# Performance work log

Hardware: AMD Instinct MI355X
Metric: run time of the kernel (lower is better)

The kernel has to match this reference:

```python
import jax, jax.numpy as jnp
import numpy as np

N, T, F, HID, HEADS, E = 10000, 6, 64, 64, 4, 160000


def gat_conv(x, W, a_src, a_dst, bias, src, dst, n, concat):
    """PyG-style GATConv (self-loops already appended to src/dst).
    x: [n, in]; W: [in, H*C]; a_src/a_dst: [H, C]; returns ([n, H*C] or [n, C], alpha [E', H])."""
    H, C = a_src.shape
    xw = (x @ W).reshape(n, H, C)
    # per-edge unnormalized attention logits
    al = (xw * a_src).sum(-1)[src] + (xw * a_dst).sum(-1)[dst]  # [E', H]
    al = jax.nn.leaky_relu(al, 0.2)
    # segment softmax over destination neighborhoods
    m = jax.ops.segment_max(al, dst, num_segments=n)
    ex = jnp.exp(al - m[dst])
    s = jax.ops.segment_sum(ex, dst, num_segments=n)
    alpha = ex / (s[dst] + 1e-16)
    out = jax.ops.segment_sum(xw[src] * alpha[:, :, None], dst, num_segments=n)  # [n, H, C]
    out = out.reshape(n, H * C) if concat else out.mean(axis=1)
    return out + bias, alpha


def setup_inputs() -> dict:
    key = jax.random.key(0)
    ks = jax.random.split(key, 12)
    sc = 0.05
    return {
        "x": jax.random.normal(ks[0], (N, T, F), jnp.float32),
        "edge_index": jax.random.randint(ks[1], (2, E), 0, N, jnp.int64),
        "W0": jax.random.normal(ks[2], (F, HID), jnp.float32) * sc,
        "a_src0": jax.random.normal(ks[3], (HEADS, HID // HEADS), jnp.float32) * sc,
        "a_dst0": jax.random.normal(ks[4], (HEADS, HID // HEADS), jnp.float32) * sc,
        "b0": jnp.zeros((HID,), jnp.float32),
        "W1": jax.random.normal(ks[5], (HID, HEADS * HID), jnp.float32) * sc,
        "a_src1": jax.random.normal(ks[6], (HEADS, HID), jnp.float32) * sc,
        "a_dst1": jax.random.normal(ks[7], (HEADS, HID), jnp.float32) * sc,
        "b1": jnp.zeros((HID,), jnp.float32),
        "ln_g": jnp.ones((HID,), jnp.float32),
        "ln_b": jnp.zeros((HID,), jnp.float32),
        "W_ih": jax.random.normal(ks[8], (3 * HID, HID), jnp.float32) * sc,
        "W_hh": jax.random.normal(ks[9], (3 * HID, HID), jnp.float32) * sc,
        "b_ih": jnp.zeros((3 * HID,), jnp.float32),
        "b_hh": jnp.zeros((3 * HID,), jnp.float32),
    }


def reference(x, edge_index, W0, a_src0, a_dst0, b0, W1, a_src1, a_dst1, b1,
              ln_g, ln_b, W_ih, W_hh, b_ih, b_hh):
    n = x.shape[0]
    loops = jnp.arange(n)
    src = jnp.concatenate([edge_index[0], loops])  # add self loops
    dst = jnp.concatenate([edge_index[1], loops])

    def gat_step(_, xt):
        h, _a = gat_conv(xt, W0, a_src0, a_dst0, b0, src, dst, n, True)
        h = jax.nn.elu(h)  # dropout is identity in eval mode
        h, alpha = gat_conv(h, W1, a_src1, a_dst1, b1, src, dst, n, False)
        h = jax.nn.elu(h)
        mu = h.mean(-1, keepdims=True)
        v = ((h - mu) ** 2).mean(-1, keepdims=True)
        h = (h - mu) / jnp.sqrt(v + 1e-5) * ln_g + ln_b
        return None, (h, alpha)

    _, (Hs, alphas) = jax.lax.scan(gat_step, None, jnp.moveaxis(x, 1, 0))  # Hs: [T, n, HID]

    def gru_step(h, xt):
        gi = xt @ W_ih.T + b_ih
        gh = h @ W_hh.T + b_hh
        ir, iz, ig = jnp.split(gi, 3, axis=-1)
        hr, hz, hg = jnp.split(gh, 3, axis=-1)
        r = jax.nn.sigmoid(ir + hr)
        z = jax.nn.sigmoid(iz + hz)
        g = jnp.tanh(ig + r * hg)
        return (1.0 - z) * g + z * h, None

    h0 = jnp.zeros((n, W_hh.shape[1]), x.dtype)
    hT, _ = jax.lax.scan(gru_step, h0, Hs)  # last GRU output == last hidden (1 layer)
    attn_edge_index = jnp.stack([src, dst])
    return hT, alphas[-1], attn_edge_index
```

## Files before the change

kernel.cpp:

```cpp
#include <hip/hip_runtime.h>
#include <hip/hip_bf16.h>
#include <cstdint>
#include <cstddef>

#define N_NODES 10000
#define T_STEPS 6
#define F_IN    64
#define HID     64
#define HEADS   4
#define E_EDGES 160000
#define EP      (E_EDGES + N_NODES)
#define TN      (T_STEPS * N_NODES)
#define NTILES  (TN / 16)

typedef __hip_bfloat16 bf16;
typedef __attribute__((ext_vector_type(8))) short short8;
typedef __attribute__((ext_vector_type(4))) float floatx4;

__device__ __forceinline__ float bfu(unsigned short s) { return __uint_as_float((unsigned)s << 16); }
__device__ __forceinline__ unsigned short f2bu(float f) {
    bf16 b = __float2bfloat16(f);
    return *(unsigned short*)&b;
}
__device__ __forceinline__ void lds_fence() {
    asm volatile("s_waitcnt lgkmcnt(0)" ::: "memory");
}


__global__ void k_count(const int* ei, int* counts) {
    int e = blockIdx.x * blockDim.x + threadIdx.x;
    if (e >= EP) return;
    int dst = (e < E_EDGES) ? ei[E_EDGES + e] : (e - E_EDGES);
    atomicAdd(&counts[dst], 1);
}

__global__ void k_scan(const int* counts, int* rowstart) {
    __shared__ int part[1024];
    int tid = threadIdx.x;
    const int chunk = (N_NODES + 1023) / 1024;
    int base = tid * chunk;
    int s = 0;
    for (int i = 0; i < chunk; i++) { int idx = base + i; if (idx < N_NODES) s += counts[idx]; }
    part[tid] = s;
    __syncthreads();
    for (int off = 1; off < 1024; off <<= 1) {
        int v = (tid >= off) ? part[tid - off] : 0;
        __syncthreads();
        part[tid] += v;
        __syncthreads();
    }
    int run = (tid == 0) ? 0 : part[tid - 1];
    for (int i = 0; i < chunk; i++) {
        int idx = base + i;
        if (idx < N_NODES) { rowstart[idx] = run; run += counts[idx]; }
    }
    if (tid == 0) rowstart[N_NODES] = EP;
}

__global__ void k_scatter(const int* ei, const int* rowstart, int* fill,
                          int* csr_src, int* csr_eid, float* out_ei) {
    int e = blockIdx.x * blockDim.x + threadIdx.x;
    if (e >= EP) return;
    int src = (e < E_EDGES) ? ei[e] : (e - E_EDGES);
    int dst = (e < E_EDGES) ? ei[E_EDGES + e] : (e - E_EDGES);
    int pos = rowstart[dst] + atomicAdd(&fill[dst], 1);
    csr_src[pos] = src;
    csr_eid[pos] = e;
    out_ei[e] = (float)src;
    out_ei[EP + e] = (float)dst;
}


__global__ __launch_bounds__(256) void k_prep(const float* __restrict__ W0,
                                              const float* __restrict__ W1,
                                              const float* __restrict__ a_src0,
                                              const float* __restrict__ a_dst0,
                                              const float* __restrict__ a_src1,
                                              const float* __restrict__ a_dst1,
                                              const float* __restrict__ W_ih,
                                              const float* __restrict__ W_hh,
                                              bf16* __restrict__ W0bt,
                                              bf16* __restrict__ W1bt,
                                              bf16* __restrict__ wihb,
                                              bf16* __restrict__ whhb,
                                              float* __restrict__ P0s,
                                              float* __restrict__ P0d,
                                              float* __restrict__ P1s,
                                              float* __restrict__ P1d) {
    int b = blockIdx.x, tid = threadIdx.x;
    if (b == 176) {
        int h = tid >> 6, k = tid & 63;
        float ps = 0.f, pd = 0.f;
        for (int c = 0; c < 64; c++) {
            float wv = W1[k * 256 + h * 64 + c];
            ps += wv * a_src1[h * 64 + c];
            pd += wv * a_dst1[h * 64 + c];
        }
        P1s[h * 64 + k] = ps;
        P1d[h * 64 + k] = pd;
        return;
    }
    if (b == 177) {
        int h = tid >> 6, k = tid & 63;
        float ps = 0.f, pd = 0.f;
        for (int c = 0; c < 16; c++) {
            float wv = W0[k * 64 + h * 16 + c];
            ps += wv * a_src0[h * 16 + c];
            pd += wv * a_dst0[h * 16 + c];
        }
        P0s[h * 64 + k] = ps;
        P0d[h * 64 + k] = pd;
        return;
    }
    int i = b * 256 + tid;
    if (i < 4096) {
        W0bt[i] = __float2bfloat16(W0[(i & 63) * 64 + (i >> 6)]);
    } else if (i < 20480) {
        int j = i - 4096; int c = j >> 8, K = j & 255;
        W1bt[j] = __float2bfloat16(W1[(K & 63) * 256 + (K >> 6) * 64 + c]);
    } else if (i < 32768) {
        wihb[i - 20480] = __float2bfloat16(W_ih[i - 20480]);
    } else {
        whhb[i - 32768] = __float2bfloat16(W_hh[i - 32768]);
    }
}

__global__ __launch_bounds__(256) void k_gemm0(const float* __restrict__ x,
                                               const bf16* __restrict__ W0bt,
                                               const float* __restrict__ P0s,
                                               const float* __restrict__ P0d,
                                               bf16* __restrict__ XW0b,
                                               float* __restrict__ ALS0,
                                               float* __restrict__ ALD0) {
    __shared__ __align__(16) bf16 wt[64 * 64];
    int tid = threadIdx.x;
    for (int i = tid; i < 512; i += 256)
        ((short8*)wt)[i] = ((const short8*)W0bt)[i];
    __syncthreads();
    int wv = tid >> 6, lane = tid & 63;
    int tile = blockIdx.x * 4 + wv;
    if (tile >= NTILES) return;
    int rb = tile * 16;
    int m = lane & 15, quad = lane >> 4;
    int row = rb + m;
    int t = row / N_NODES, n = row - t * N_NODES;
    const float* xr = x + ((size_t)n * T_STEPS + t) * F_IN + quad * 8;
    short8 a0, a1;
#pragma unroll
    for (int j = 0; j < 8; j++) {
        a0[j] = (short)f2bu(xr[j]);
        a1[j] = (short)f2bu(xr[32 + j]);
    }
    floatx4 acc[4];
#pragma unroll
    for (int ct = 0; ct < 4; ct++) {
        short8 bb0 = *(const short8*)(wt + (ct * 16 + m) * 64 + quad * 8);
        short8 bb1 = *(const short8*)(wt + (ct * 16 + m) * 64 + 32 + quad * 8);
        floatx4 a = {0.f, 0.f, 0.f, 0.f};
        a = __builtin_amdgcn_mfma_f32_16x16x32_bf16(a0, bb0, a, 0, 0, 0);
        a = __builtin_amdgcn_mfma_f32_16x16x32_bf16(a1, bb1, a, 0, 0, 0);
        acc[ct] = a;
    }
    short8 p0, p1;
#pragma unroll
    for (int j = 0; j < 8; j++) {
        int k0 = quad * 8 + j, k1 = 32 + quad * 8 + j;
        float v0 = 0.f, v1 = 0.f;
        if (m < 4)      { v0 = P0s[m * 64 + k0];       v1 = P0s[m * 64 + k1]; }
        else if (m < 8) { v0 = P0d[(m - 4) * 64 + k0]; v1 = P0d[(m - 4) * 64 + k1]; }
        p0[j] = (short)f2bu(v0);
        p1[j] = (short)f2bu(v1);
    }
    floatx4 ac5 = {0.f, 0.f, 0.f, 0.f};
    ac5 = __builtin_amdgcn_mfma_f32_16x16x32_bf16(a0, p0, ac5, 0, 0, 0);
    ac5 = __builtin_amdgcn_mfma_f32_16x16x32_bf16(a1, p1, ac5, 0, 0, 0);
#pragma unroll
    for (int ct = 0; ct < 4; ct++)
#pragma unroll
        for (int r = 0; r < 4; r++)
            XW0b[(size_t)(rb + quad * 4 + r) * 64 + ct * 16 + m] = __float2bfloat16(acc[ct][r]);
#pragma unroll
    for (int r = 0; r < 4; r++) {
        int orow = rb + quad * 4 + r;
        if (m < 4)      ALS0[orow * 4 + m] = ac5[r];
        else if (m < 8) ALD0[orow * 4 + (m - 4)] = ac5[r];
    }
}

__global__ __launch_bounds__(256) void k_fused0(const int* __restrict__ rowst,
                                                const int* __restrict__ csr_src,
                                                const bf16* __restrict__ XW0b,
                                                const float* __restrict__ ALS0,
                                                const float* __restrict__ ALD0,
                                                const float* __restrict__ b0,
                                                const float* __restrict__ P1s,
                                                const float* __restrict__ P1d,
                                                bf16* __restrict__ H0b,
                                                float* __restrict__ ALS1,
                                                float* __restrict__ ALD1) {
    __shared__ float exv[4][4][65][4];
    __shared__ int   srcs[4][4][68];
    int tid = threadIdx.x;
    int wv = tid >> 6, lane = tid & 63;
    int sub = lane >> 4, il = lane & 15;
    int wid = (blockIdx.x * 4 + wv) * 4 + sub;
    int t = wid / N_NODES, n = wid - t * N_NODES;
    int rs = rowst[n], re = rowst[n + 1];
    int deg = re - rs;
    int tb = t * N_NODES;
    int hsel = il >> 2;
    float4 ad = *(const float4*)(ALD0 + (size_t)wid * 4);
    float s0 = 0.f, s1 = 0.f, s2 = 0.f, s3 = 0.f;
    float a0 = 0.f, a1 = 0.f, a2 = 0.f, a3 = 0.f;
    float i0, i1, i2, i3;
    const bf16* hrow = XW0b + (size_t)tb * 64 + il * 4;

    if (deg <= 64) {
        int srcv[4];
#pragma unroll
        for (int b = 0; b < 4; b++) {
            int idx = b * 16 + il;
            srcv[b] = csr_src[idx < deg ? rs + idx : rs];
        }
        float4 asv[4];
#pragma unroll
        for (int b = 0; b < 4; b++)
            asv[b] = *(const float4*)(ALS0 + (size_t)(tb + srcv[b]) * 4);
#pragma unroll
        for (int b = 0; b < 4; b++) {
            int idx = b * 16 + il;
            bool valid = idx < deg;
            float l0 = asv[b].x + ad.x; l0 = l0 > 0.f ? l0 : 0.2f * l0;
            float l1 = asv[b].y + ad.y; l1 = l1 > 0.f ? l1 : 0.2f * l1;
            float l2 = asv[b].z + ad.z; l2 = l2 > 0.f ? l2 : 0.2f * l2;
            float l3 = asv[b].w + ad.w; l3 = l3 > 0.f ? l3 : 0.2f * l3;
            float e0 = valid ? __expf(fminf(l0, 80.f)) : 0.f;
            float e1 = valid ? __expf(fminf(l1, 80.f)) : 0.f;
            float e2 = valid ? __expf(fminf(l2, 80.f)) : 0.f;
            float e3 = valid ? __expf(fminf(l3, 80.f)) : 0.f;
            s0 += e0; s1 += e1; s2 += e2; s3 += e3;
            float4 ex4; ex4.x = e0; ex4.y = e1; ex4.z = e2; ex4.w = e3;
            *(float4*)&exv[wv][sub][idx][0] = ex4;
            srcs[wv][sub][idx] = srcv[b];
        }
#pragma unroll
        for (int o = 1; o <= 8; o <<= 1) {
            s0 += __shfl_xor(s0, o, 64); s1 += __shfl_xor(s1, o, 64);
            s2 += __shfl_xor(s2, o, 64); s3 += __shfl_xor(s3, o, 64);
        }
        i0 = 1.f / (s0 + 1e-16f); i1 = 1.f / (s1 + 1e-16f);
        i2 = 1.f / (s2 + 1e-16f); i3 = 1.f / (s3 + 1e-16f);
        lds_fence();
        int k = 0;
        for (; k + 4 <= deg; k += 4) {
            float axq[4]; int sxq[4];
#pragma unroll
            for (int j = 0; j < 4; j++) {
                axq[j] = exv[wv][sub][k + j][hsel];
                sxq[j] = srcs[wv][sub][k + j];
            }
            ushort4 uq[4];
#pragma unroll
            for (int j = 0; j < 4; j++)
                uq[j] = *(const ushort4*)(hrow + (size_t)sxq[j] * 64);
#pragma unroll
            for (int j = 0; j < 4; j++) {
                a0 += axq[j] * bfu(uq[j].x); a1 += axq[j] * bfu(uq[j].y);
                a2 += axq[j] * bfu(uq[j].z); a3 += axq[j] * bfu(uq[j].w);
            }
        }
        for (; k < deg; k++) {
            float aex = exv[wv][sub][k][hsel];
            int sx = srcs[wv][sub][k];
            ushort4 u = *(const ushort4*)(hrow + (size_t)sx * 64);
            a0 += aex * bfu(u.x); a1 += aex * bfu(u.y);
            a2 += aex * bfu(u.z); a3 += aex * bfu(u.w);
        }
    } else {
        for (int idx = il; idx < deg; idx += 16) {
            int src = csr_src[rs + idx];
            float4 as = *(const float4*)(ALS0 + (size_t)(tb + src) * 4);
            float l0 = as.x + ad.x; l0 = l0 > 0.f ? l0 : 0.2f * l0; s0 += __expf(fminf(l0, 80.f));
            float l1 = as.y + ad.y; l1 = l1 > 0.f ? l1 : 0.2f * l1; s1 += __expf(fminf(l1, 80.f));
            float l2 = as.z + ad.z; l2 = l2 > 0.f ? l2 : 0.2f * l2; s2 += __expf(fminf(l2, 80.f));
            float l3 = as.w + ad.w; l3 = l3 > 0.f ? l3 : 0.2f * l3; s3 += __expf(fminf(l3, 80.f));
        }
#pragma unroll
        for (int o = 1; o <= 8; o <<= 1) {
            s0 += __shfl_xor(s0, o, 64); s1 += __shfl_xor(s1, o, 64);
            s2 += __shfl_xor(s2, o, 64); s3 += __shfl_xor(s3, o, 64);
        }
        i0 = 1.f / (s0 + 1e-16f); i1 = 1.f / (s1 + 1e-16f);
        i2 = 1.f / (s2 + 1e-16f); i3 = 1.f / (s3 + 1e-16f);
        for (int cb = 0; cb < deg; cb += 64) {
            int cend = min(64, deg - cb);
            lds_fence();
            for (int q = 0; q < 64; q += 16) {
                int idx = q + il;
                bool valid = idx < cend;
                int src = csr_src[valid ? (rs + cb + idx) : rs];
                float4 as = *(const float4*)(ALS0 + (size_t)(tb + src) * 4);
                float l0 = as.x + ad.x; l0 = l0 > 0.f ? l0 : 0.2f * l0;
                float l1 = as.y + ad.y; l1 = l1 > 0.f ? l1 : 0.2f * l1;
                float l2 = as.z + ad.z; l2 = l2 > 0.f ? l2 : 0.2f * l2;
                float l3 = as.w + ad.w; l3 = l3 > 0.f ? l3 : 0.2f * l3;
                float4 ex4;
                ex4.x = valid ? __expf(fminf(l0, 80.f)) : 0.f;
                ex4.y = valid ? __expf(fminf(l1, 80.f)) : 0.f;
                ex4.z = valid ? __expf(fminf(l2, 80.f)) : 0.f;
                ex4.w = valid ? __expf(fminf(l3, 80.f)) : 0.f;
                *(float4*)&exv[wv][sub][idx][0] = ex4;
                srcs[wv][sub][idx] = src;
            }
            lds_fence();
            for (int k = 0; k < cend; k++) {
                float aex = exv[wv][sub][k][hsel];
                int sx = srcs[wv][sub][k];
                ushort4 u = *(const ushort4*)(hrow + (size_t)sx * 64);
                a0 += aex * bfu(u.x); a1 += aex * bfu(u.y);
                a2 += aex * bfu(u.z); a3 += aex * bfu(u.w);
            }
        }
    }
    float ih = (hsel == 0) ? i0 : (hsel == 1) ? i1 : (hsel == 2) ? i2 : i3;
    float4 bv = *(const float4*)(b0 + il * 4);
    float v0 = a0 * ih + bv.x; v0 = v0 > 0.f ? v0 : (__expf(v0) - 1.f);
    float v1 = a1 * ih + bv.y; v1 = v1 > 0.f ? v1 : (__expf(v1) - 1.f);
    float v2 = a2 * ih + bv.z; v2 = v2 > 0.f ? v2 : (__expf(v2) - 1.f);
    float v3 = a3 * ih + bv.w; v3 = v3 > 0.f ? v3 : (__expf(v3) - 1.f);
    ushort4 o4;
    o4.x = f2bu(v0); o4.y = f2bu(v1); o4.z = f2bu(v2); o4.w = f2bu(v3);
    *(ushort4*)(H0b + (size_t)wid * 64 + il * 4) = o4;

    float ps[4], pd[4];
#pragma unroll
    for (int h = 0; h < 4; h++) {
        float4 s4 = *(const float4*)(P1s + h * 64 + il * 4);
        float4 d4 = *(const float4*)(P1d + h * 64 + il * 4);
        ps[h] = v0 * s4.x + v1 * s4.y + v2 * s4.z + v3 * s4.w;
        pd[h] = v0 * d4.x + v1 * d4.y + v2 * d4.z + v3 * d4.w;
    }
#pragma unroll
    for (int o = 1; o <= 8; o <<= 1) {
#pragma unroll
        for (int h = 0; h < 4; h++) {
            ps[h] += __shfl_xor(ps[h], o, 64);
            pd[h] += __shfl_xor(pd[h], o, 64);
        }
    }
    if (il == 0) {
        float4 w1; w1.x = ps[0]; w1.y = ps[1]; w1.z = ps[2]; w1.w = ps[3];
        *(float4*)(ALS1 + (size_t)wid * 4) = w1;
        float4 w2; w2.x = pd[0]; w2.y = pd[1]; w2.z = pd[2]; w2.w = pd[3];
        *(float4*)(ALD1 + (size_t)wid * 4) = w2;
    }
}

__global__ __launch_bounds__(256) void k_fused1(const int* __restrict__ rowst,
                                                const int* __restrict__ csr_src,
                                                const int* __restrict__ csr_eid,
                                                const bf16* __restrict__ H0b,
                                                const float* __restrict__ ALS1,
                                                const float* __restrict__ ALD1,
                                                const bf16* __restrict__ W1bt,
                                                const float* __restrict__ b1,
                                                const float* __restrict__ ln_g,
                                                const float* __restrict__ ln_b,
                                                bf16* __restrict__ HSb,
                                                float* __restrict__ out_alpha) {
    __shared__ __align__(16) union SM {
        struct { float exv[4][4][65][4]; int srcs[4][4][68]; } p;
        struct { bf16 ast[16][264]; float ost[16][68]; } q;
    } sm;
    int tid = threadIdx.x;
    int wv = tid >> 6, lane = tid & 63;
    int sub = lane >> 4, il = lane & 15;
    int wid = (blockIdx.x * 4 + wv) * 4 + sub;
    int t = wid / N_NODES, n = wid - t * N_NODES;
    int rs = rowst[n], re = rowst[n + 1];
    int deg = re - rs;
    int tb = t * N_NODES;
    bool do_out = (t == T_STEPS - 1);
    float4 ad = *(const float4*)(ALD1 + (size_t)wid * 4);
    float s0 = 0.f, s1 = 0.f, s2 = 0.f, s3 = 0.f;
    float acc[4][4];
#pragma unroll
    for (int hh = 0; hh < 4; hh++)
#pragma unroll
        for (int j = 0; j < 4; j++) acc[hh][j] = 0.f;
    float i0, i1, i2, i3;
    const bf16* hrow = H0b + (size_t)tb * 64 + il * 4;

    if (deg <= 64) {
        int srcv[4];
#pragma unroll
        for (int b = 0; b < 4; b++) {
            int idx = b * 16 + il;
            srcv[b] = csr_src[idx < deg ? rs + idx : rs];
        }
        float4 asv[4];
#pragma unroll
        for (int b = 0; b < 4; b++)
            asv[b] = *(const float4*)(ALS1 + (size_t)(tb + srcv[b]) * 4);
#pragma unroll
        for (int b = 0; b < 4; b++) {
            int idx = b * 16 + il;
            bool valid = idx < deg;
            float l0 = asv[b].x + ad.x; l0 = l0 > 0.f ? l0 : 0.2f * l0;
            float l1 = asv[b].y + ad.y; l1 = l1 > 0.f ? l1 : 0.2f * l1;
            float l2 = asv[b].z + ad.z; l2 = l2 > 0.f ? l2 : 0.2f * l2;
            float l3 = asv[b].w + ad.w; l3 = l3 > 0.f ? l3 : 0.2f * l3;
            float e0 = valid ? __expf(fminf(l0, 80.f)) : 0.f;
            float e1 = valid ? __expf(fminf(l1, 80.f)) : 0.f;
            float e2 = valid ? __expf(fminf(l2, 80.f)) : 0.f;
            float e3 = valid ? __expf(fminf(l3, 80.f)) : 0.f;
            s0 += e0; s1 += e1; s2 += e2; s3 += e3;
            float4 ex4; ex4.x = e0; ex4.y = e1; ex4.z = e2; ex4.w = e3;
            *(float4*)&sm.p.exv[wv][sub][idx][0] = ex4;
            sm.p.srcs[wv][sub][idx] = srcv[b];
        }
#pragma unroll
        for (int o = 1; o <= 8; o <<= 1) {
            s0 += __shfl_xor(s0, o, 64); s1 += __shfl_xor(s1, o, 64);
            s2 += __shfl_xor(s2, o, 64); s3 += __shfl_xor(s3, o, 64);
        }
        i0 = 1.f / (s0 + 1e-16f); i1 = 1.f / (s1 + 1e-16f);
        i2 = 1.f / (s2 + 1e-16f); i3 = 1.f / (s3 + 1e-16f);
        lds_fence();
        if (do_out) {
            for (int b = 0; b < deg; b += 16) {
                int idx = b + il;
                if (idx < deg) {
                    int eid = csr_eid[rs + idx];
                    float4 ex4 = *(const float4*)&sm.p.exv[wv][sub][idx][0];
                    float4 o4;
                    o4.x = ex4.x * i0; o4.y = ex4.y * i1;
                    o4.z = ex4.z * i2; o4.w = ex4.w * i3;
                    *(float4*)(out_alpha + (size_t)eid * 4) = o4;
                }
            }
        }
        int k = 0;
        for (; k + 4 <= deg; k += 4) {
            float4 exq[4]; int sxq[4];
#pragma unroll
            for (int j = 0; j < 4; j++) {
                exq[j] = *(const float4*)&sm.p.exv[wv][sub][k + j][0];
                sxq[j] = sm.p.srcs[wv][sub][k + j];
            }
            ushort4 uq[4];
#pragma unroll
            for (int j = 0; j < 4; j++)
                uq[j] = *(const ushort4*)(hrow + (size_t)sxq[j] * 64);
#pragma unroll
            for (int j = 0; j < 4; j++) {
                float x0 = bfu(uq[j].x), x1 = bfu(uq[j].y), x2 = bfu(uq[j].z), x3 = bfu(uq[j].w);
                acc[0][0] += exq[j].x * x0; acc[0][1] += exq[j].x * x1; acc[0][2] += exq[j].x * x2; acc[0][3] += exq[j].x * x3;
                acc[1][0] += exq[j].y * x0; acc[1][1] += exq[j].y * x1; acc[1][2] += exq[j].y * x2; acc[1][3] += exq[j].y * x3;
                acc[2][0] += exq[j].z * x0; acc[2][1] += exq[j].z * x1; acc[2][2] += exq[j].z * x2; acc[2][3] += exq[j].z * x3;
                acc[3][0] += exq[j].w * x0; acc[3][1] += exq[j].w * x1; acc[3][2] += exq[j].w * x2; acc[3][3] += exq[j].w * x3;
            }
        }
        for (; k < deg; k++) {
            float4 ex = *(const float4*)&sm.p.exv[wv][sub][k][0];
            int sx = sm.p.srcs[wv][sub][k];
            ushort4 u = *(const ushort4*)(hrow + (size_t)sx * 64);
            float x0 = bfu(u.x), x1 = bfu(u.y), x2 = bfu(u.z), x3 = bfu(u.w);
            acc[0][0] += ex.x * x0; acc[0][1] += ex.x * x1; acc[0][2] += ex.x * x2; acc[0][3] += ex.x * x3;
            acc[1][0] += ex.y * x0; acc[1][1] += ex.y * x1; acc[1][2] += ex.y * x2; acc[1][3] += ex.y * x3;
            acc[2][0] += ex.z * x0; acc[2][1] += ex.z * x1; acc[2][2] += ex.z * x2; acc[2][3] += ex.z * x3;
            acc[3][0] += ex.w * x0; acc[3][1] += ex.w * x1; acc[3][2] += ex.w * x2; acc[3][3] += ex.w * x3;
        }
    } else {
        for (int idx = il; idx < deg; idx += 16) {
            int src = csr_src[rs + idx];
            float4 as = *(const float4*)(ALS1 + (size_t)(tb + src) * 4);
            float l0 = as.x + ad.x; l0 = l0 > 0.f ? l0 : 0.2f * l0; s0 += __expf(fminf(l0, 80.f));
            float l1 = as.y + ad.y; l1 = l1 > 0.f ? l1 : 0.2f * l1; s1 += __expf(fminf(l1, 80.f));
            float l2 = as.z + ad.z; l2 = l2 > 0.f ? l2 : 0.2f * l2; s2 += __expf(fminf(l2, 80.f));
            float l3 = as.w + ad.w; l3 = l3 > 0.f ? l3 : 0.2f * l3; s3 += __expf(fminf(l3, 80.f));
        }
#pragma unroll
        for (int o = 1; o <= 8; o <<= 1) {
            s0 += __shfl_xor(s0, o, 64); s1 += __shfl_xor(s1, o, 64);
            s2 += __shfl_xor(s2, o, 64); s3 += __shfl_xor(s3, o, 64);
        }
        i0 = 1.f / (s0 + 1e-16f); i1 = 1.f / (s1 + 1e-16f);
        i2 = 1.f / (s2 + 1e-16f); i3 = 1.f / (s3 + 1e-16f);
        for (int cb = 0; cb < deg; cb += 64) {
            int cend = min(64, deg - cb);
            lds_fence();
            for (int q = 0; q < 64; q += 16) {
                int idx = q + il;
                bool valid = idx < cend;
                int e = rs + cb + idx;
                int src = csr_src[valid ? e : rs];
                float4 as = *(const float4*)(ALS1 + (size_t)(tb + src) * 4);
                float l0 = as.x + ad.x; l0 = l0 > 0.f ? l0 : 0.2f * l0;
                float l1 = as.y + ad.y; l1 = l1 > 0.f ? l1 : 0.2f * l1;
                float l2 = as.z + ad.z; l2 = l2 > 0.f ? l2 : 0.2f * l2;
                float l3 = as.w + ad.w; l3 = l3 > 0.f ? l3 : 0.2f * l3;
                float e0 = valid ? __expf(fminf(l0, 80.f)) : 0.f;
                float e1 = valid ? __expf(fminf(l1, 80.f)) : 0.f;
                float e2 = valid ? __expf(fminf(l2, 80.f)) : 0.f;
                float e3 = valid ? __expf(fminf(l3, 80.f)) : 0.f;
                float4 ex4; ex4.x = e0; ex4.y = e1; ex4.z = e2; ex4.w = e3;
                *(float4*)&sm.p.exv[wv][sub][idx][0] = ex4;
                sm.p.srcs[wv][sub][idx] = src;
                if (do_out && valid) {
                    int eid = csr_eid[e];
                    float4 o4;
                    o4.x = e0 * i0; o4.y = e1 * i1; o4.z = e2 * i2; o4.w = e3 * i3;
                    *(float4*)(out_alpha + (size_t)eid * 4) = o4;
                }
            }
            lds_fence();
            for (int k = 0; k < cend; k++) {
                float4 ex = *(const float4*)&sm.p.exv[wv][sub][k][0];
                int sx = sm.p.srcs[wv][sub][k];
                ushort4 u = *(const ushort4*)(hrow + (size_t)sx * 64);
                float x0 = bfu(u.x), x1 = bfu(u.y), x2 = bfu(u.z), x3 = bfu(u.w);
                acc[0][0] += ex.x * x0; acc[0][1] += ex.x * x1; acc[0][2] += ex.x * x2; acc[0][3] += ex.x * x3;
                acc[1][0] += ex.y * x0; acc[1][1] += ex.y * x1; acc[1][2] += ex.y * x2; acc[1][3] += ex.y * x3;
                acc[2][0] += ex.z * x0; acc[2][1] += ex.z * x1; acc[2][2] += ex.z * x2; acc[2][3] += ex.z * x3;
                acc[3][0] += ex.w * x0; acc[3][1] += ex.w * x1; acc[3][2] += ex.w * x2; acc[3][3] += ex.w * x3;
            }
        }
    }
    float iv[4] = { i0, i1, i2, i3 };

    __syncthreads();
    int r_local = wv * 4 + sub;
#pragma unroll
    for (int hh = 0; hh < 4; hh++) {
        ushort4 o4;
        o4.x = f2bu(acc[hh][0] * iv[hh]); o4.y = f2bu(acc[hh][1] * iv[hh]);
        o4.z = f2bu(acc[hh][2] * iv[hh]); o4.w = f2bu(acc[hh][3] * iv[hh]);
        *(ushort4*)&sm.q.ast[r_local][hh * 64 + il * 4] = o4;
    }
    __syncthreads();
    int m = il, quad = sub;
    floatx4 ga = {0.f, 0.f, 0.f, 0.f};
    const bf16* wrow = W1bt + (size_t)(wv * 16 + m) * 256 + quad * 8;
#pragma unroll
    for (int kb = 0; kb < 8; kb++) {
        short8 afk = *(const short8*)&sm.q.ast[m][kb * 32 + quad * 8];
        short8 bfk = *(const short8*)(wrow + kb * 32);
        ga = __builtin_amdgcn_mfma_f32_16x16x32_bf16(afk, bfk, ga, 0, 0, 0);
    }
#pragma unroll
    for (int r = 0; r < 4; r++)
        sm.q.ost[quad * 4 + r][wv * 16 + m] = ga[r];
    __syncthreads();
    int row = wv * 4 + quad;
    float4 vv = *(const float4*)&sm.q.ost[row][m * 4];
    float4 bb = *(const float4*)(b1 + m * 4);
    float v0 = vv.x * 0.25f + bb.x; v0 = v0 > 0.f ? v0 : (__expf(v0) - 1.f);
    float v1 = vv.y * 0.25f + bb.y; v1 = v1 > 0.f ? v1 : (__expf(v1) - 1.f);
    float v2 = vv.z * 0.25f + bb.z; v2 = v2 > 0.f ? v2 : (__expf(v2) - 1.f);
    float v3 = vv.w * 0.25f + bb.w; v3 = v3 > 0.f ? v3 : (__expf(v3) - 1.f);
    float s = v0 + v1 + v2 + v3;
#pragma unroll
    for (int o = 1; o <= 8; o <<= 1) s += __shfl_xor(s, o, 64);
    float mu = s * (1.f / 64.f);
    float d0 = v0 - mu, d1 = v1 - mu, d2 = v2 - mu, d3 = v3 - mu;
    float qv = d0 * d0 + d1 * d1 + d2 * d2 + d3 * d3;
#pragma unroll
    for (int o = 1; o <= 8; o <<= 1) qv += __shfl_xor(qv, o, 64);
    float rinv = rsqrtf(qv * (1.f / 64.f) + 1e-5f);
    float4 gg = *(const float4*)(ln_g + m * 4);
    float4 lb = *(const float4*)(ln_b + m * 4);
    ushort4 ho;
    ho.x = f2bu(d0 * rinv * gg.x + lb.x);
    ho.y = f2bu(d1 * rinv * gg.y + lb.y);
    ho.z = f2bu(d2 * rinv * gg.z + lb.z);
    ho.w = f2bu(d3 * rinv * gg.w + lb.w);
    *(ushort4*)(HSb + (size_t)(blockIdx.x * 16 + row) * 64 + m * 4) = ho;
}

__global__ __launch_bounds__(256) void k_gru(const bf16* __restrict__ HSb,
                                             const bf16* __restrict__ wihb,
                                             const float* __restrict__ b_ih,
                                             const bf16* __restrict__ whhb,
                                             const float* __restrict__ b_hh,
                                             float* __restrict__ outh) {
    __shared__ __align__(16) bf16 hbuf[16 * 72];
    int tid = threadIdx.x;
    int wv = tid >> 6, lane = tid & 63;
    int rb = blockIdx.x * 16;
    int m = lane & 15, quad = lane >> 4;
    int fb = wv * 16;
    const int rowR = (fb + m) * 64, rowZ = (64 + fb + m) * 64, rowG = (128 + fb + m) * 64;
    short8 Br0 = *(const short8*)(wihb + rowR + quad * 8);
    short8 Br1 = *(const short8*)(wihb + rowR + 32 + quad * 8);
    short8 Bz0 = *(const short8*)(wihb + rowZ + quad * 8);
    short8 Bz1 = *(const short8*)(wihb + rowZ + 32 + quad * 8);
    short8 Bg0 = *(const short8*)(wihb + rowG + quad * 8);
    short8 Bg1 = *(const short8*)(wihb + rowG + 32 + quad * 8);
    short8 Cr0 = *(const short8*)(whhb + rowR + quad * 8);
    short8 Cr1 = *(const short8*)(whhb + rowR + 32 + quad * 8);
    short8 Cz0 = *(const short8*)(whhb + rowZ + quad * 8);
    short8 Cz1 = *(const short8*)(whhb + rowZ + 32 + quad * 8);
    short8 Cg0 = *(const short8*)(whhb + rowG + quad * 8);
    short8 Cg1 = *(const short8*)(whhb + rowG + 32 + quad * 8);
    float biR = b_ih[fb + m], biZ = b_ih[64 + fb + m], biG = b_ih[128 + fb + m];
    float bhR = b_hh[fb + m], bhZ = b_hh[64 + fb + m], bhG = b_hh[128 + fb + m];
    float hprev[4] = {0.f, 0.f, 0.f, 0.f};

    for (int t = 0; t < T_STEPS; t++) {
        const bf16* xr = HSb + ((size_t)t * N_NODES + rb + m) * 64;
        short8 ax0 = *(const short8*)(xr + quad * 8);
        short8 ax1 = *(const short8*)(xr + 32 + quad * 8);
        short8 ah0, ah1;
        if (t > 0) {
            ah0 = *(const short8*)(hbuf + m * 72 + quad * 8);
            ah1 = *(const short8*)(hbuf + m * 72 + 32 + quad * 8);
        }
        __syncthreads();
        floatx4 aR = {0.f, 0.f, 0.f, 0.f}, aZ = {0.f, 0.f, 0.f, 0.f};
        floatx4 aGi = {0.f, 0.f, 0.f, 0.f}, aGh = {0.f, 0.f, 0.f, 0.f};
        aR = __builtin_amdgcn_mfma_f32_16x16x32_bf16(ax0, Br0, aR, 0, 0, 0);
        aR = __builtin_amdgcn_mfma_f32_16x16x32_bf16(ax1, Br1, aR, 0, 0, 0);
        aZ = __builtin_amdgcn_mfma_f32_16x16x32_bf16(ax0, Bz0, aZ, 0, 0, 0);
        aZ = __builtin_amdgcn_mfma_f32_16x16x32_bf16(ax1, Bz1, aZ, 0, 0, 0);
        aGi = __builtin_amdgcn_mfma_f32_16x16x32_bf16(ax0, Bg0, aGi, 0, 0, 0);
        aGi = __builtin_amdgcn_mfma_f32_16x16x32_bf16(ax1, Bg1, aGi, 0, 0, 0);
        if (t > 0) {
            aR = __builtin_amdgcn_mfma_f32_16x16x32_bf16(ah0, Cr0, aR, 0, 0, 0);
            aR = __builtin_amdgcn_mfma_f32_16x16x32_bf16(ah1, Cr1, aR, 0, 0, 0);
            aZ = __builtin_amdgcn_mfma_f32_16x16x32_bf16(ah0, Cz0, aZ, 0, 0, 0);
            aZ = __builtin_amdgcn_mfma_f32_16x16x32_bf16(ah1, Cz1, aZ, 0, 0, 0);
            aGh = __builtin_amdgcn_mfma_f32_16x16x32_bf16(ah0, Cg0, aGh, 0, 0, 0);
            aGh = __builtin_amdgcn_mfma_f32_16x16x32_bf16(ah1, Cg1, aGh, 0, 0, 0);
        }
#pragma unroll
        for (int r = 0; r < 4; r++) {
            float rr = 1.f / (1.f + __expf(-(aR[r] + biR + bhR)));
            float z  = 1.f / (1.f + __expf(-(aZ[r] + biZ + bhZ)));
            float g  = tanhf(aGi[r] + biG + rr * (aGh[r] + bhG));
            hprev[r] = (1.f - z) * g + z * hprev[r];
        }
        if (t < T_STEPS - 1) {
#pragma unroll
            for (int r = 0; r < 4; r++)
                hbuf[(quad * 4 + r) * 72 + fb + m] = __float2bfloat16(hprev[r]);
            __syncthreads();
        }
    }
#pragma unroll
    for (int r = 0; r < 4; r++)
        outh[(size_t)(rb + quad * 4 + r) * 64 + fb + m] = hprev[r];
}


extern "C" void kernel_launch(void* const* d_in, const int* in_sizes, int n_in,
                              void* d_out, int out_size, void* d_ws, size_t ws_size,
                              hipStream_t stream) {
    const float* x      = (const float*)d_in[0];
    const int*   ei     = (const int*)d_in[1];
    const float* W0     = (const float*)d_in[2];
    const float* a_src0 = (const float*)d_in[3];
    const float* a_dst0 = (const float*)d_in[4];
    const float* b0     = (const float*)d_in[5];
    const float* W1     = (const float*)d_in[6];
    const float* a_src1 = (const float*)d_in[7];
    const float* a_dst1 = (const float*)d_in[8];
    const float* b1     = (const float*)d_in[9];
    const float* ln_g   = (const float*)d_in[10];
    const float* ln_b   = (const float*)d_in[11];
    const float* W_ih   = (const float*)d_in[12];
    const float* W_hh   = (const float*)d_in[13];
    const float* b_ih   = (const float*)d_in[14];
    const float* b_hh   = (const float*)d_in[15];
    float* out = (float*)d_out;

    char* w = (char*)d_ws;
    size_t off = 0;
    auto take = [&](size_t bytes) -> void* {
        void* p = w + off;
        off = (off + bytes + 255) & ~(size_t)255;
        return p;
    };
    int*   counts  = (int*)take(N_NODES * 4);
    int*   fill    = (int*)take(N_NODES * 4);
    size_t zero_bytes = off;
    int*   rowst   = (int*)take((N_NODES + 1) * 4);
    int*   csr_src = (int*)take((size_t)EP * 4);
    int*   csr_eid = (int*)take((size_t)EP * 4);
    bf16*  XW0b    = (bf16*)take((size_t)TN * 64 * 2);
    float* ALS0    = (float*)take((size_t)TN * 4 * 4);
    float* ALD0    = (float*)take((size_t)TN * 4 * 4);
    bf16*  H0b     = (bf16*)take((size_t)TN * 64 * 2);
    float* P0s     = (float*)take(256 * 4);
    float* P0d     = (float*)take(256 * 4);
    float* P1s     = (float*)take(256 * 4);
    float* P1d     = (float*)take(256 * 4);
    float* ALS1    = (float*)take((size_t)TN * 4 * 4);
    float* ALD1    = (float*)take((size_t)TN * 4 * 4);
    bf16*  HSb     = (bf16*)take((size_t)TN * 64 * 2);
    bf16*  W0bt    = (bf16*)take(4096 * 2);
    bf16*  W1bt    = (bf16*)take(16384 * 2);
    bf16*  wihb    = (bf16*)take(12288 * 2);
    bf16*  whhb    = (bf16*)take(12288 * 2);
    (void)ws_size; (void)in_sizes; (void)n_in; (void)out_size;

    const int B = 256;
    float* out_ei = out + (size_t)N_NODES * HID + (size_t)EP * HEADS;

    hipMemsetAsync(counts, 0, zero_bytes, stream);
    k_count<<<(EP + B - 1) / B, B, 0, stream>>>(ei, counts);
    k_scan<<<1, 1024, 0, stream>>>(counts, rowst);
    k_scatter<<<(EP + B - 1) / B, B, 0, stream>>>(ei, rowst, fill, csr_src, csr_eid, out_ei);
    k_prep<<<178, B, 0, stream>>>(W0, W1, a_src0, a_dst0, a_src1, a_dst1, W_ih, W_hh,
                                  W0bt, W1bt, wihb, whhb, P0s, P0d, P1s, P1d);

    const int GT = (NTILES + 3) / 4;
    k_gemm0<<<GT, B, 0, stream>>>(x, W0bt, P0s, P0d, XW0b, ALS0, ALD0);
    k_fused0<<<TN / 16, B, 0, stream>>>(rowst, csr_src, XW0b, ALS0, ALD0, b0,
                                        P1s, P1d, H0b, ALS1, ALD1);

    k_fused1<<<TN / 16, B, 0, stream>>>(rowst, csr_src, csr_eid, H0b, ALS1, ALD1,
                                        W1bt, b1, ln_g, ln_b, HSb,
                                        out + (size_t)N_NODES * HID);

    k_gru<<<N_NODES / 16, B, 0, stream>>>(HSb, wihb, b_ih, whhb, b_hh, out);
}
```

Before: 228.7 us.

## Interleave timesteps per node, trim edge batches, fuse count into prep

The fused GAT kernels now map each group of consecutive subgroups to the same node across its six timesteps, so CSR row reads for a node are shared and hit cache. Edge batches in the small-degree path are bounded by the maximum degree within the wavefront instead of always four batches, which skips unused gathers and exps. Source indices in LDS shrink to 16-bit. The edge-count kernel is merged into the prep kernel to drop a launch. The output row remapping in fused1 adds some integer division, and the 16-bit indices only hold while node ids stay below 65536.

After: 227.2 us. About the same (-0.6%).

```diff
diff --git a/kernel.cpp b/kernel.cpp
--- a/kernel.cpp
+++ b/kernel.cpp
@@ -26,13 +26,6 @@
     asm volatile("s_waitcnt lgkmcnt(0)" ::: "memory");
 }
 
-
-__global__ void k_count(const int* ei, int* counts) {
-    int e = blockIdx.x * blockDim.x + threadIdx.x;
-    if (e >= EP) return;
-    int dst = (e < E_EDGES) ? ei[E_EDGES + e] : (e - E_EDGES);
-    atomicAdd(&counts[dst], 1);
-}
 
 __global__ void k_scan(const int* counts, int* rowstart) {
     __shared__ int part[1024];
@@ -79,6 +72,8 @@
                                               const float* __restrict__ a_dst1,
                                               const float* __restrict__ W_ih,
                                               const float* __restrict__ W_hh,
+                                              const int* __restrict__ ei,
+                                              int* __restrict__ counts,
                                               bf16* __restrict__ W0bt,
                                               bf16* __restrict__ W1bt,
                                               bf16* __restrict__ wihb,
@@ -88,6 +83,14 @@
                                               float* __restrict__ P1s,
                                               float* __restrict__ P1d) {
     int b = blockIdx.x, tid = threadIdx.x;
+    if (b >= 178) {
+        int e = (b - 178) * 256 + tid;
+        if (e < EP) {
+            int dst = (e < E_EDGES) ? ei[E_EDGES + e] : (e - E_EDGES);
+            atomicAdd(&counts[dst], 1);
+        }
+        return;
+    }
     if (b == 176) {
         int h = tid >> 6, k = tid & 63;
         float ps = 0.f, pd = 0.f;
@@ -199,49 +202,46 @@
                                                 float* __restrict__ ALS1,
                                                 float* __restrict__ ALD1) {
     __shared__ float exv[4][4][65][4];
-    __shared__ int   srcs[4][4][68];
+    __shared__ unsigned short srcs[4][4][66];
     int tid = threadIdx.x;
     int wv = tid >> 6, lane = tid & 63;
     int sub = lane >> 4, il = lane & 15;
-    int wid = (blockIdx.x * 4 + wv) * 4 + sub;
-    int t = wid / N_NODES, n = wid - t * N_NODES;
+    int s = (blockIdx.x * 4 + wv) * 4 + sub;
+    int n = s / T_STEPS, t = s - n * T_STEPS;
+    int idx = t * N_NODES + n;
     int rs = rowst[n], re = rowst[n + 1];
     int deg = re - rs;
     int tb = t * N_NODES;
     int hsel = il >> 2;
-    float4 ad = *(const float4*)(ALD0 + (size_t)wid * 4);
+    float4 ad = *(const float4*)(ALD0 + (size_t)idx * 4);
     float s0 = 0.f, s1 = 0.f, s2 = 0.f, s3 = 0.f;
     float a0 = 0.f, a1 = 0.f, a2 = 0.f, a3 = 0.f;
     float i0, i1, i2, i3;
     const bf16* hrow = XW0b + (size_t)tb * 64 + il * 4;
 
+    int mdf = (deg <= 64) ? deg : 0;
+    mdf = max(mdf, __shfl_xor(mdf, 16, 64));
+    mdf = max(mdf, __shfl_xor(mdf, 32, 64));
+    int nbf = (mdf + 15) >> 4;
+
     if (deg <= 64) {
-        int srcv[4];
-#pragma unroll
-        for (int b = 0; b < 4; b++) {
-            int idx = b * 16 + il;
-            srcv[b] = csr_src[idx < deg ? rs + idx : rs];
-        }
-        float4 asv[4];
-#pragma unroll
-        for (int b = 0; b < 4; b++)
-            asv[b] = *(const float4*)(ALS0 + (size_t)(tb + srcv[b]) * 4);
-#pragma unroll
-        for (int b = 0; b < 4; b++) {
-            int idx = b * 16 + il;
-            bool valid = idx < deg;
-            float l0 = asv[b].x + ad.x; l0 = l0 > 0.f ? l0 : 0.2f * l0;
-            float l1 = asv[b].y + ad.y; l1 = l1 > 0.f ? l1 : 0.2f * l1;
-            float l2 = asv[b].z + ad.z; l2 = l2 > 0.f ? l2 : 0.2f * l2;
-            float l3 = asv[b].w + ad.w; l3 = l3 > 0.f ? l3 : 0.2f * l3;
+        for (int b = 0; b < nbf; b++) {
+            int idxe = b * 16 + il;
+            bool valid = idxe < deg;
+            int src = csr_src[valid ? rs + idxe : rs];
+            float4 as = *(const float4*)(ALS0 + (size_t)(tb + src) * 4);
+            float l0 = as.x + ad.x; l0 = l0 > 0.f ? l0 : 0.2f * l0;
+            float l1 = as.y + ad.y; l1 = l1 > 0.f ? l1 : 0.2f * l1;
+            float l2 = as.z + ad.z; l2 = l2 > 0.f ? l2 : 0.2f * l2;
+            float l3 = as.w + ad.w; l3 = l3 > 0.f ? l3 : 0.2f * l3;
             float e0 = valid ? __expf(fminf(l0, 80.f)) : 0.f;
             float e1 = valid ? __expf(fminf(l1, 80.f)) : 0.f;
             float e2 = valid ? __expf(fminf(l2, 80.f)) : 0.f;
             float e3 = valid ? __expf(fminf(l3, 80.f)) : 0.f;
             s0 += e0; s1 += e1; s2 += e2; s3 += e3;
             float4 ex4; ex4.x = e0; ex4.y = e1; ex4.z = e2; ex4.w = e3;
-            *(float4*)&exv[wv][sub][idx][0] = ex4;
-            srcs[wv][sub][idx] = srcv[b];
+            *(float4*)&exv[wv][sub][idxe][0] = ex4;
+            srcs[wv][sub][idxe] = (unsigned short)src;
         }
 #pragma unroll
         for (int o = 1; o <= 8; o <<= 1) {
@@ -277,8 +277,8 @@
             a2 += aex * bfu(u.z); a3 += aex * bfu(u.w);
         }
     } else {
-        for (int idx = il; idx < deg; idx += 16) {
-            int src = csr_src[rs + idx];
+        for (int idxe = il; idxe < deg; idxe += 16) {
+            int src = csr_src[rs + idxe];
             float4 as = *(const float4*)(ALS0 + (size_t)(tb + src) * 4);
             float l0 = as.x + ad.x; l0 = l0 > 0.f ? l0 : 0.2f * l0; s0 += __expf(fminf(l0, 80.f));
             float l1 = as.y + ad.y; l1 = l1 > 0.f ? l1 : 0.2f * l1; s1 += __expf(fminf(l1, 80.f));
@@ -296,9 +296,9 @@
             int cend = min(64, deg - cb);
             lds_fence();
             for (int q = 0; q < 64; q += 16) {
-                int idx = q + il;
-                bool valid = idx < cend;
-                int src = csr_src[valid ? (rs + cb + idx) : rs];
+                int idxe = q + il;
+                bool valid = idxe < cend;
+                int src = csr_src[valid ? (rs + cb + idxe) : rs];
                 float4 as = *(const float4*)(ALS0 + (size_t)(tb + src) * 4);
                 float l0 = as.x + ad.x; l0 = l0 > 0.f ? l0 : 0.2f * l0;
                 float l1 = as.y + ad.y; l1 = l1 > 0.f ? l1 : 0.2f * l1;
@@ -309,8 +309,8 @@
                 ex4.y = valid ? __expf(fminf(l1, 80.f)) : 0.f;
                 ex4.z = valid ? __expf(fminf(l2, 80.f)) : 0.f;
                 ex4.w = valid ? __expf(fminf(l3, 80.f)) : 0.f;
-                *(float4*)&exv[wv][sub][idx][0] = ex4;
-                srcs[wv][sub][idx] = src;
+                *(float4*)&exv[wv][sub][idxe][0] = ex4;
+                srcs[wv][sub][idxe] = (unsigned short)src;
             }
             lds_fence();
             for (int k = 0; k < cend; k++) {
@@ -330,7 +330,7 @@
     float v3 = a3 * ih + bv.w; v3 = v3 > 0.f ? v3 : (__expf(v3) - 1.f);
     ushort4 o4;
     o4.x = f2bu(v0); o4.y = f2bu(v1); o4.z = f2bu(v2); o4.w = f2bu(v3);
-    *(ushort4*)(H0b + (size_t)wid * 64 + il * 4) = o4;
+    *(ushort4*)(H0b + (size_t)idx * 64 + il * 4) = o4;
 
     float ps[4], pd[4];
 #pragma unroll
@@ -350,9 +350,9 @@
     }
     if (il == 0) {
         float4 w1; w1.x = ps[0]; w1.y = ps[1]; w1.z = ps[2]; w1.w = ps[3];
-        *(float4*)(ALS1 + (size_t)wid * 4) = w1;
+        *(float4*)(ALS1 + (size_t)idx * 4) = w1;
         float4 w2; w2.x = pd[0]; w2.y = pd[1]; w2.z = pd[2]; w2.w = pd[3];
-        *(float4*)(ALD1 + (size_t)wid * 4) = w2;
+        *(float4*)(ALD1 + (size_t)idx * 4) = w2;
     }
 }
 
@@ -369,19 +369,20 @@
                                                 bf16* __restrict__ HSb,
                                                 float* __restrict__ out_alpha) {
     __shared__ __align__(16) union SM {
-        struct { float exv[4][4][65][4]; int srcs[4][4][68]; } p;
+        struct { float exv[4][4][65][4]; unsigned short srcs[4][4][66]; } p;
         struct { bf16 ast[16][264]; float ost[16][68]; } q;
     } sm;
     int tid = threadIdx.x;
     int wv = tid >> 6, lane = tid & 63;
     int sub = lane >> 4, il = lane & 15;
-    int wid = (blockIdx.x * 4 + wv) * 4 + sub;
-    int t = wid / N_NODES, n = wid - t * N_NODES;
+    int s = (blockIdx.x * 4 + wv) * 4 + sub;
+    int n = s / T_STEPS, t = s - n * T_STEPS;
+    int idx = t * N_NODES + n;
     int rs = rowst[n], re = rowst[n + 1];
     int deg = re - rs;
     int tb = t * N_NODES;
     bool do_out = (t == T_STEPS - 1);
-    float4 ad = *(const float4*)(ALD1 + (size_t)wid * 4);
+    float4 ad = *(const float4*)(ALD1 + (size_t)idx * 4);
     float s0 = 0.f, s1 = 0.f, s2 = 0.f, s3 = 0.f;
     float acc[4][4];
 #pragma unroll
@@ -391,33 +392,29 @@
     float i0, i1, i2, i3;
     const bf16* hrow = H0b + (size_t)tb * 64 + il * 4;
 
+    int mdf = (deg <= 64) ? deg : 0;
+    mdf = max(mdf, __shfl_xor(mdf, 16, 64));
+    mdf = max(mdf, __shfl_xor(mdf, 32, 64));
+    int nbf = (mdf + 15) >> 4;
+
     if (deg <= 64) {
-        int srcv[4];
-#pragma unroll
-        for (int b = 0; b < 4; b++) {
-            int idx = b * 16 + il;
-            srcv[b] = csr_src[idx < deg ? rs + idx : rs];
-        }
-        float4 asv[4];
-#pragma unroll
-        for (int b = 0; b < 4; b++)
-            asv[b] = *(const float4*)(ALS1 + (size_t)(tb + srcv[b]) * 4);
-#pragma unroll
-        for (int b = 0; b < 4; b++) {
-            int idx = b * 16 + il;
-            bool valid = idx < deg;
-            float l0 = asv[b].x + ad.x; l0 = l0 > 0.f ? l0 : 0.2f * l0;
-            float l1 = asv[b].y + ad.y; l1 = l1 > 0.f ? l1 : 0.2f * l1;
-            float l2 = asv[b].z + ad.z; l2 = l2 > 0.f ? l2 : 0.2f * l2;
-            float l3 = asv[b].w + ad.w; l3 = l3 > 0.f ? l3 : 0.2f * l3;
+        for (int b = 0; b < nbf; b++) {
+            int idxe = b * 16 + il;
+            bool valid = idxe < deg;
+            int src = csr_src[valid ? rs + idxe : rs];
+            float4 as = *(const float4*)(ALS1 + (size_t)(tb + src) * 4);
+            float l0 = as.x + ad.x; l0 = l0 > 0.f ? l0 : 0.2f * l0;
+            float l1 = as.y + ad.y; l1 = l1 > 0.f ? l1 : 0.2f * l1;
+            float l2 = as.z + ad.z; l2 = l2 > 0.f ? l2 : 0.2f * l2;
+            float l3 = as.w + ad.w; l3 = l3 > 0.f ? l3 : 0.2f * l3;
             float e0 = valid ? __expf(fminf(l0, 80.f)) : 0.f;
             float e1 = valid ? __expf(fminf(l1, 80.f)) : 0.f;
             float e2 = valid ? __expf(fminf(l2, 80.f)) : 0.f;
             float e3 = valid ? __expf(fminf(l3, 80.f)) : 0.f;
             s0 += e0; s1 += e1; s2 += e2; s3 += e3;
             float4 ex4; ex4.x = e0; ex4.y = e1; ex4.z = e2; ex4.w = e3;
-            *(float4*)&sm.p.exv[wv][sub][idx][0] = ex4;
-            sm.p.srcs[wv][sub][idx] = srcv[b];
+            *(float4*)&sm.p.exv[wv][sub][idxe][0] = ex4;
+            sm.p.srcs[wv][sub][idxe] = (unsigned short)src;
         }
 #pragma unroll
         for (int o = 1; o <= 8; o <<= 1) {
@@ -429,10 +426,10 @@
         lds_fence();
         if (do_out) {
             for (int b = 0; b < deg; b += 16) {
-                int idx = b + il;
-                if (idx < deg) {
-                    int eid = csr_eid[rs + idx];
-                    float4 ex4 = *(const float4*)&sm.p.exv[wv][sub][idx][0];
+                int idxe = b + il;
+                if (idxe < deg) {
+                    int eid = csr_eid[rs + idxe];
+                    float4 ex4 = *(const float4*)&sm.p.exv[wv][sub][idxe][0];
                     float4 o4;
                     o4.x = ex4.x * i0; o4.y = ex4.y * i1;
                     o4.z = ex4.z * i2; o4.w = ex4.w * i3;
@@ -472,8 +469,8 @@
             acc[3][0] += ex.w * x0; acc[3][1] += ex.w * x1; acc[3][2] += ex.w * x2; acc[3][3] += ex.w * x3;
         }
     } else {
-        for (int idx = il; idx < deg; idx += 16) {
-            int src = csr_src[rs + idx];
+        for (int idxe = il; idxe < deg; idxe += 16) {
+            int src = csr_src[rs + idxe];
             float4 as = *(const float4*)(ALS1 + (size_t)(tb + src) * 4);
             float l0 = as.x + ad.x; l0 = l0 > 0.f ? l0 : 0.2f * l0; s0 += __expf(fminf(l0, 80.f));
             float l1 = as.y + ad.y; l1 = l1 > 0.f ? l1 : 0.2f * l1; s1 += __expf(fminf(l1, 80.f));
@@ -491,9 +488,9 @@
             int cend = min(64, deg - cb);
             lds_fence();
             for (int q = 0; q < 64; q += 16) {
-                int idx = q + il;
-                bool valid = idx < cend;
-                int e = rs + cb + idx;
+                int idxe = q + il;
+                bool valid = idxe < cend;
+                int e = rs + cb + idxe;
                 int src = csr_src[valid ? e : rs];
                 float4 as = *(const float4*)(ALS1 + (size_t)(tb + src) * 4);
                 float l0 = as.x + ad.x; l0 = l0 > 0.f ? l0 : 0.2f * l0;
@@ -505,8 +502,8 @@
                 float e2 = valid ? __expf(fminf(l2, 80.f)) : 0.f;
                 float e3 = valid ? __expf(fminf(l3, 80.f)) : 0.f;
                 float4 ex4; ex4.x = e0; ex4.y = e1; ex4.z = e2; ex4.w = e3;
-                *(float4*)&sm.p.exv[wv][sub][idx][0] = ex4;
-                sm.p.srcs[wv][sub][idx] = src;
+                *(float4*)&sm.p.exv[wv][sub][idxe][0] = ex4;
+                sm.p.srcs[wv][sub][idxe] = (unsigned short)src;
                 if (do_out && valid) {
                     int eid = csr_eid[e];
                     float4 o4;
@@ -559,10 +556,10 @@
     float v1 = vv.y * 0.25f + bb.y; v1 = v1 > 0.f ? v1 : (__expf(v1) - 1.f);
     float v2 = vv.z * 0.25f + bb.z; v2 = v2 > 0.f ? v2 : (__expf(v2) - 1.f);
     float v3 = vv.w * 0.25f + bb.w; v3 = v3 > 0.f ? v3 : (__expf(v3) - 1.f);
-    float s = v0 + v1 + v2 + v3;
-#pragma unroll
-    for (int o = 1; o <= 8; o <<= 1) s += __shfl_xor(s, o, 64);
-    float mu = s * (1.f / 64.f);
+    float sv = v0 + v1 + v2 + v3;
+#pragma unroll
+    for (int o = 1; o <= 8; o <<= 1) sv += __shfl_xor(sv, o, 64);
+    float mu = sv * (1.f / 64.f);
     float d0 = v0 - mu, d1 = v1 - mu, d2 = v2 - mu, d3 = v3 - mu;
     float qv = d0 * d0 + d1 * d1 + d2 * d2 + d3 * d3;
 #pragma unroll
@@ -575,7 +572,9 @@
     ho.y = f2bu(d1 * rinv * gg.y + lb.y);
     ho.z = f2bu(d2 * rinv * gg.z + lb.z);
     ho.w = f2bu(d3 * rinv * gg.w + lb.w);
-    *(ushort4*)(HSb + (size_t)(blockIdx.x * 16 + row) * 64 + m * 4) = ho;
+    int s_row = blockIdx.x * 16 + row;
+    int n_r = s_row / T_STEPS, t_r = s_row - n_r * T_STEPS;
+    *(ushort4*)(HSb + (size_t)(t_r * N_NODES + n_r) * 64 + m * 4) = ho;
 }
 
 __global__ __launch_bounds__(256) void k_gru(const bf16* __restrict__ HSb,
@@ -708,11 +707,12 @@
     float* out_ei = out + (size_t)N_NODES * HID + (size_t)EP * HEADS;
 
     hipMemsetAsync(counts, 0, zero_bytes, stream);
-    k_count<<<(EP + B - 1) / B, B, 0, stream>>>(ei, counts);
+    const int PREPG = 178 + (EP + B - 1) / B;
+    k_prep<<<PREPG, B, 0, stream>>>(W0, W1, a_src0, a_dst0, a_src1, a_dst1, W_ih, W_hh,
+                                    ei, counts,
+                                    W0bt, W1bt, wihb, whhb, P0s, P0d, P1s, P1d);
     k_scan<<<1, 1024, 0, stream>>>(counts, rowst);
     k_scatter<<<(EP + B - 1) / B, B, 0, stream>>>(ei, rowst, fill, csr_src, csr_eid, out_ei);
-    k_prep<<<178, B, 0, stream>>>(W0, W1, a_src0, a_dst0, a_src1, a_dst1, W_ih, W_hh,
-                                  W0bt, W1bt, wihb, whhb, P0s, P0d, P1s, P1d);
 
     const int GT = (NTILES + 3) / 4;
     k_gemm0<<<GT, B, 0, stream>>>(x, W0bt, P0s, P0d, XW0b, ALS0, ALD0);
```
